# Kernel tuning notes

Hardware: AMD Instinct MI355X
Metric: run time of the kernel (lower is better)

## Reference

```python
import jax, jax.numpy as jnp
import numpy as np

B, S, D_IN = 2, 2048, 1024
H, DA, DH = 16, 64, 64          # num_heads, attention_dim, head_dim (linear_hidden_dim)
EMBED = 1024
KSIZE = 1


def causal_conv1d(x_bsc, w):
    """x_bsc: (B,S,Cin); w: (Cout,Cin,K). Left-pad K-1 -> causal. Returns (B,Cout,S)."""
    k = w.shape[-1]
    x_bcs = jnp.transpose(x_bsc, (0, 2, 1))
    x_bcs = jnp.pad(x_bcs, ((0, 0), (0, 0), (k - 1, 0)))
    return jax.lax.conv_general_dilated(
        x_bcs, w, window_strides=(1,), padding='VALID',
        dimension_numbers=('NCH', 'OIH', 'NCH'))


def setup_inputs() -> dict:
    key = jax.random.key(0)
    ks = jax.random.split(key, 7)
    x = jax.random.normal(ks[0], (B, S, D_IN), dtype=jnp.float32)
    # causal mask: 1 where attended, 0 where masked (masked_fill where ==0)
    attn_mask = jnp.tril(jnp.ones((S, S), dtype=jnp.int32))[None, None]  # (1,1,S,S)
    wq = 0.02 * jax.random.normal(ks[1], (H * DA, D_IN, KSIZE), dtype=jnp.float32)
    wk = 0.02 * jax.random.normal(ks[2], (H * DA, D_IN, KSIZE), dtype=jnp.float32)
    wv = 0.02 * jax.random.normal(ks[3], (H * DH, D_IN, KSIZE), dtype=jnp.float32)
    w_out = 0.02 * jax.random.normal(ks[4], (EMBED, H * DH), dtype=jnp.float32)
    b_out = 0.02 * jax.random.normal(ks[5], (EMBED,), dtype=jnp.float32)
    return {"x": x, "attn_mask": attn_mask, "wq": wq, "wk": wk, "wv": wv,
            "w_out": w_out, "b_out": b_out}


def reference(x, attn_mask, wq, wk, wv, w_out, b_out):
    b, s, _ = x.shape
    scale = DH ** (-0.5)  # NOTE: torch code scales by head_dim, not attention_dim
    q = causal_conv1d(x, wq)  # (B, H*DA, S)
    k = causal_conv1d(x, wk)  # (B, H*DA, S)
    v = causal_conv1d(x, wv)  # (B, H*DH, S)
    q = q.reshape(b, H, DA, s).transpose(0, 1, 3, 2)  # (B,H,S,DA)
    k = k.reshape(b, H, DA, s).transpose(0, 1, 3, 2)
    v = v.reshape(b, H, DH, s).transpose(0, 1, 3, 2)  # (B,H,S,DH)
    scores = scale * jnp.einsum('bhnd,bhmd->bhnm', q, k)
    scores = jnp.where(attn_mask == 0, -jnp.inf, scores)
    probs = jax.nn.softmax(scores, axis=-1)
    context = jnp.einsum('bhnm,bhmd->bhnd', probs, v)  # (B,H,S,DH)
    context = context.transpose(0, 2, 1, 3).reshape(b, s, H * DH)
    return context @ w_out.T + b_out
```

## Files before the change

### kernel.cpp

```cpp
#include <hip/hip_runtime.h>
#include <math.h>


typedef __bf16 bf16;
typedef __bf16 bf16x8 __attribute__((ext_vector_type(8)));
typedef __bf16 bf16x4 __attribute__((ext_vector_type(4)));
typedef float  f32x4  __attribute__((ext_vector_type(4)));

#define MFMA16(a, b, c) __builtin_amdgcn_mfma_f32_16x16x32_bf16((a), (b), (c), 0, 0, 0)

__device__ __forceinline__ void gll16(const void* g, void* l) {
    __builtin_amdgcn_global_load_lds(
        (__attribute__((address_space(1))) unsigned int*)g,
        (__attribute__((address_space(3))) unsigned int*)l, 16, 0, 0);
}

__global__ __launch_bounds__(256) void cvt_all_kernel(
    const float* __restrict__ x,  const float* __restrict__ wq,
    const float* __restrict__ wk, const float* __restrict__ wv,
    const float* __restrict__ wo,
    bf16* __restrict__ xb,  bf16* __restrict__ wqb, bf16* __restrict__ wkb,
    bf16* __restrict__ wvb, bf16* __restrict__ wob)
{
    const int blk = blockIdx.x;
    const float* src; bf16* dst; int off; float scale = 1.f;
    if (blk < 4096)      { src = x;  dst = xb;  off = blk * 1024; }
    else if (blk < 5120) { src = wq; dst = wqb; off = (blk - 4096) * 1024; scale = 0.125f; }
    else if (blk < 6144) { src = wk; dst = wkb; off = (blk - 5120) * 1024; }
    else if (blk < 7168) { src = wv; dst = wvb; off = (blk - 6144) * 1024; }
    else                 { src = wo; dst = wob; off = (blk - 7168) * 1024; }
    const int i = off + threadIdx.x * 4;
    f32x4 v = *(const f32x4*)(src + i);
    bf16x4 o;
    o[0] = (bf16)(v[0] * scale); o[1] = (bf16)(v[1] * scale);
    o[2] = (bf16)(v[2] * scale); o[3] = (bf16)(v[3] * scale);
    *(bf16x4*)(dst + i) = o;
}

__global__ __launch_bounds__(256, 3) void qkv_mfma_kernel(
    const bf16* __restrict__ xb, const bf16* __restrict__ wqb,
    const bf16* __restrict__ wkb, const bf16* __restrict__ wvb,
    bf16* __restrict__ Qb, bf16* __restrict__ Kb, bf16* __restrict__ Vtb)
{
    __shared__ bf16 As[2][128 * 32];
    __shared__ bf16 Bs[2][128 * 32];
    const int mt = blockIdx.x;
    const int nt = blockIdx.y;
    const int which = nt >> 3;
    const bf16* Wm = (which == 0) ? wqb : (which == 1) ? wkb : wvb;

    const int t = threadIdx.x;
    const int w = t >> 6, lane = t & 63, quad = lane >> 4, l16 = lane & 15;
    const int wm = (w >> 1) * 64, wn = (w & 1) * 64;
    const int srow = lane >> 2;
    const int scol = (lane & 3) * 8;

    const bf16* Ab = xb + ((size_t)(mt * 128) + srow) * 1024 + scol;
    const bf16* Bb = Wm + ((size_t)((nt & 7) * 128) + srow) * 1024 + scol;

    f32x4 acc[4][4];
    #pragma unroll
    for (int i = 0; i < 4; i++)
        #pragma unroll
        for (int j = 0; j < 4; j++)
            #pragma unroll
            for (int r = 0; r < 4; r++) acc[i][j][r] = 0.f;

    gll16(Ab + (size_t)(w * 16) * 1024,       As[0] + w * 512);
    gll16(Ab + (size_t)((w + 4) * 16) * 1024, As[0] + (w + 4) * 512);
    gll16(Bb + (size_t)(w * 16) * 1024,       Bs[0] + w * 512);
    gll16(Bb + (size_t)((w + 4) * 16) * 1024, Bs[0] + (w + 4) * 512);

    for (int it = 0; it < 32; it++) {
        const int cur = it & 1, nxt = cur ^ 1;
        __syncthreads();
        if (it < 31) {
            const int kn = it * 32 + 32;
            gll16(Ab + (size_t)(w * 16) * 1024 + kn,       As[nxt] + w * 512);
            gll16(Ab + (size_t)((w + 4) * 16) * 1024 + kn, As[nxt] + (w + 4) * 512);
            gll16(Bb + (size_t)(w * 16) * 1024 + kn,       Bs[nxt] + w * 512);
            gll16(Bb + (size_t)((w + 4) * 16) * 1024 + kn, Bs[nxt] + (w + 4) * 512);
        }
        bf16x8 af[4], bfr[4];
        #pragma unroll
        for (int i = 0; i < 4; i++)
            af[i] = *(const bf16x8*)&As[cur][(wm + i * 16 + l16) * 32 + quad * 8];
        #pragma unroll
        for (int j = 0; j < 4; j++)
            bfr[j] = *(const bf16x8*)&Bs[cur][(wn + j * 16 + l16) * 32 + quad * 8];
        #pragma unroll
        for (int i = 0; i < 4; i++)
            #pragma unroll
            for (int j = 0; j < 4; j++)
                acc[i][j] = MFMA16(af[i], bfr[j], acc[i][j]);
    }

    const int nbase = (nt & 7) * 128 + wn;
    #pragma unroll
    for (int i = 0; i < 4; i++) {
        #pragma unroll
        for (int r = 0; r < 4; r++) {
            const int m = mt * 128 + wm + i * 16 + quad * 4 + r;
            const int bb = m >> 11, s = m & 2047;
            #pragma unroll
            for (int j = 0; j < 4; j++) {
                const int n = nbase + j * 16 + l16;
                const int h = n >> 6, d = n & 63;
                bf16 val = (bf16)acc[i][j][r];
                if (which == 0)
                    Qb[(((size_t)(bb * 16 + h)) * 2048 + s) * 64 + d] = val;
                else if (which == 1)
                    Kb[(((size_t)(bb * 16 + h)) * 2048 + s) * 64 + d] = val;
                else
                    Vtb[(((size_t)(bb * 16 + h)) * 64 + d) * 2048 + s] = val;
            }
        }
    }
}

__global__ __launch_bounds__(256, 2) void attn_mfma_kernel(
    const bf16* __restrict__ Qb, const bf16* __restrict__ Kb,
    const bf16* __restrict__ Vtb, bf16* __restrict__ ctxb)
{
    __shared__ bf16 Qs[128 * 64];
    __shared__ bf16 Ks[2][64 * 64];
    __shared__ bf16 Vts[2][64 * 64];
    __shared__ bf16 Pl[4][32 * 72];

    const int id = blockIdx.x;
    const int bh = id & 31;
    const int g = id >> 5;
    const int qt = (g < 8) ? g : (23 - g);
    const int h = bh & 15, b = bh >> 4;
    const int t = threadIdx.x;
    const int w = t >> 6, lane = t & 63, quad = lane >> 4, l16 = lane & 15;
    const int sr = lane >> 3, sc = lane & 7;

    const size_t hb = (size_t)(b * 16 + h);
    const bf16* Qh = Qb + hb * (2048 * 64);
    const bf16* Kh = Kb + hb * (2048 * 64);
    const bf16* Vh = Vtb + hb * (64 * 2048);

    #pragma unroll
    for (int j = 0; j < 4; j++) {
        const int c = w + 4 * j;
        const int r0 = c * 8 + sr;
        gll16(Qh + (size_t)(qt * 128 + r0) * 64 + (sc ^ sr) * 8, Qs + c * 512);
    }
    {
        const int r0 = w * 8 + sr, r1 = (w + 4) * 8 + sr;
        gll16(Kh + (size_t)r0 * 64 + (sc ^ sr) * 8, Ks[0] + w * 512);
        gll16(Kh + (size_t)r1 * 64 + (sc ^ sr) * 8, Ks[0] + (w + 4) * 512);
        gll16(Vh + (size_t)r0 * 2048 + (sc ^ sr) * 8, Vts[0] + w * 512);
        gll16(Vh + (size_t)r1 * 2048 + (sc ^ sr) * 8, Vts[0] + (w + 4) * 512);
    }
    __syncthreads();

    bf16x8 aq[2][2];
    #pragma unroll
    for (int rt = 0; rt < 2; rt++) {
        const int row = w * 32 + rt * 16 + l16;
        aq[rt][0] = *(const bf16x8*)&Qs[row * 64 + ((quad)     ^ (row & 7)) * 8];
        aq[rt][1] = *(const bf16x8*)&Qs[row * 64 + ((quad + 4) ^ (row & 7)) * 8];
    }

    bf16x8 ones;
    #pragma unroll
    for (int i = 0; i < 8; i++) ones[i] = (bf16)1.0f;

    f32x4 o_acc[2][4], l_acc[2];
    #pragma unroll
    for (int rt = 0; rt < 2; rt++) {
        #pragma unroll
        for (int r = 0; r < 4; r++) l_acc[rt][r] = 0.f;
        #pragma unroll
        for (int dt = 0; dt < 4; dt++)
            #pragma unroll
            for (int r = 0; r < 4; r++) o_acc[rt][dt][r] = 0.f;
    }

    const int ktmax = 2 * qt + 1;
    for (int kt = 0; kt <= ktmax; kt++) {
        const int cur = kt & 1, nxt = cur ^ 1;
        __syncthreads();
        if (kt < ktmax) {
            const int kn = kt + 1;
            const int r0 = w * 8 + sr, r1 = (w + 4) * 8 + sr;
            gll16(Kh + (size_t)(kn * 64 + r0) * 64 + (sc ^ sr) * 8, Ks[nxt] + w * 512);
            gll16(Kh + (size_t)(kn * 64 + r1) * 64 + (sc ^ sr) * 8, Ks[nxt] + (w + 4) * 512);
            gll16(Vh + (size_t)r0 * 2048 + kn * 64 + (sc ^ sr) * 8, Vts[nxt] + w * 512);
            gll16(Vh + (size_t)r1 * 2048 + kn * 64 + (sc ^ sr) * 8, Vts[nxt] + (w + 4) * 512);
        }

        f32x4 sacc[2][4];
        #pragma unroll
        for (int rt = 0; rt < 2; rt++)
            #pragma unroll
            for (int tt = 0; tt < 4; tt++)
                #pragma unroll
                for (int r = 0; r < 4; r++) sacc[rt][tt][r] = 0.f;
        #pragma unroll
        for (int tt = 0; tt < 4; tt++) {
            const int krow = tt * 16 + l16;
            bf16x8 bk0 = *(const bf16x8*)&Ks[cur][krow * 64 + ((quad)     ^ (krow & 7)) * 8];
            bf16x8 bk1 = *(const bf16x8*)&Ks[cur][krow * 64 + ((quad + 4) ^ (krow & 7)) * 8];
            #pragma unroll
            for (int rt = 0; rt < 2; rt++) {
                sacc[rt][tt] = MFMA16(aq[rt][0], bk0, sacc[rt][tt]);
                sacc[rt][tt] = MFMA16(aq[rt][1], bk1, sacc[rt][tt]);
            }
        }

        const bool diag = (kt >= 2 * qt);
        #pragma unroll
        for (int rt = 0; rt < 2; rt++)
            #pragma unroll
            for (int r = 0; r < 4; r++) {
                const int rw = rt * 16 + quad * 4 + r;
                const int qrow = qt * 128 + w * 32 + rw;
                #pragma unroll
                for (int tt = 0; tt < 4; tt++) {
                    float p = __expf(sacc[rt][tt][r]);
                    if (diag && (kt * 64 + tt * 16 + l16) > qrow) p = 0.f;
                    Pl[w][rw * 72 + tt * 16 + l16] = (bf16)p;
                }
            }

        bf16x8 bv[4][2];
        #pragma unroll
        for (int dt = 0; dt < 4; dt++) {
            const int drow = dt * 16 + l16;
            bv[dt][0] = *(const bf16x8*)&Vts[cur][drow * 64 + ((quad)     ^ (drow & 7)) * 8];
            bv[dt][1] = *(const bf16x8*)&Vts[cur][drow * 64 + ((quad + 4) ^ (drow & 7)) * 8];
        }
        #pragma unroll
        for (int rt = 0; rt < 2; rt++) {
            bf16x8 ap0 = *(const bf16x8*)&Pl[w][(rt * 16 + l16) * 72 + quad * 8];
            bf16x8 ap1 = *(const bf16x8*)&Pl[w][(rt * 16 + l16) * 72 + 32 + quad * 8];
            l_acc[rt] = MFMA16(ap0, ones, l_acc[rt]);
            l_acc[rt] = MFMA16(ap1, ones, l_acc[rt]);
            #pragma unroll
            for (int dt = 0; dt < 4; dt++) {
                o_acc[rt][dt] = MFMA16(ap0, bv[dt][0], o_acc[rt][dt]);
                o_acc[rt][dt] = MFMA16(ap1, bv[dt][1], o_acc[rt][dt]);
            }
        }
    }

    #pragma unroll
    for (int rt = 0; rt < 2; rt++)
        #pragma unroll
        for (int r = 0; r < 4; r++) {
            const float inv = 1.f / l_acc[rt][r];
            const int s = qt * 128 + w * 32 + rt * 16 + quad * 4 + r;
            #pragma unroll
            for (int dt = 0; dt < 4; dt++)
                ctxb[((size_t)(b * 2048 + s)) * 1024 + h * 64 + dt * 16 + l16] =
                    (bf16)(o_acc[rt][dt][r] * inv);
        }
}

__global__ __launch_bounds__(256, 2) void oproj_mfma_kernel(
    const bf16* __restrict__ ctxb, const bf16* __restrict__ wob,
    const float* __restrict__ b_out, float* __restrict__ out)
{
    __shared__ bf16 As[2][64 * 32];
    __shared__ bf16 Bs[2][128 * 32];
    const int mt = blockIdx.x;
    const int nt = blockIdx.y;
    const int t = threadIdx.x;
    const int w = t >> 6, lane = t & 63, quad = lane >> 4, l16 = lane & 15;
    const int srow = lane >> 2;
    const int scol = (lane & 3) * 8;

    const bf16* Ab = ctxb + (size_t)(mt * 64 + srow) * 1024 + scol;
    const bf16* Bb = wob + (size_t)(nt * 128 + srow) * 1024 + scol;

    f32x4 acc[8];
    #pragma unroll
    for (int j = 0; j < 8; j++)
        #pragma unroll
        for (int r = 0; r < 4; r++) acc[j][r] = 0.f;

    gll16(Ab + (size_t)(w * 16) * 1024,       As[0] + w * 512);
    gll16(Bb + (size_t)(w * 16) * 1024,       Bs[0] + w * 512);
    gll16(Bb + (size_t)((w + 4) * 16) * 1024, Bs[0] + (w + 4) * 512);

    for (int it = 0; it < 32; it++) {
        const int cur = it & 1, nxt = cur ^ 1;
        __syncthreads();
        if (it < 31) {
            const int kn = it * 32 + 32;
            gll16(Ab + (size_t)(w * 16) * 1024 + kn,       As[nxt] + w * 512);
            gll16(Bb + (size_t)(w * 16) * 1024 + kn,       Bs[nxt] + w * 512);
            gll16(Bb + (size_t)((w + 4) * 16) * 1024 + kn, Bs[nxt] + (w + 4) * 512);
        }
        bf16x8 af = *(const bf16x8*)&As[cur][(w * 16 + l16) * 32 + quad * 8];
        #pragma unroll
        for (int j = 0; j < 8; j++) {
            bf16x8 bfr = *(const bf16x8*)&Bs[cur][(j * 16 + l16) * 32 + quad * 8];
            acc[j] = MFMA16(af, bfr, acc[j]);
        }
    }

    #pragma unroll
    for (int j = 0; j < 8; j++)
        #pragma unroll
        for (int r = 0; r < 4; r++) {
            const int m = mt * 64 + w * 16 + quad * 4 + r;
            const int n = nt * 128 + j * 16 + l16;
            out[(size_t)m * 1024 + n] = acc[j][r] + b_out[n];
        }
}

extern "C" void kernel_launch(void* const* d_in, const int* in_sizes, int n_in,
                              void* d_out, int out_size, void* d_ws, size_t ws_size,
                              hipStream_t stream)
{
    const float* x     = (const float*)d_in[0];
    const float* wq    = (const float*)d_in[2];
    const float* wk    = (const float*)d_in[3];
    const float* wv    = (const float*)d_in[4];
    const float* w_out = (const float*)d_in[5];
    const float* b_out = (const float*)d_in[6];
    float* out = (float*)d_out;

    char* ws = (char*)d_ws;
    bf16* xb   = (bf16*)(ws);
    bf16* wqb  = (bf16*)(ws + (8u  << 20));
    bf16* wkb  = (bf16*)(ws + (10u << 20));
    bf16* wvb  = (bf16*)(ws + (12u << 20));
    bf16* wob  = (bf16*)(ws + (14u << 20));
    bf16* Qb   = (bf16*)(ws + (16u << 20));
    bf16* Kb   = (bf16*)(ws + (24u << 20));
    bf16* Vtb  = (bf16*)(ws + (32u << 20));
    bf16* ctxb = (bf16*)(ws + (40u << 20));

    cvt_all_kernel<<<8192, 256, 0, stream>>>(x, wq, wk, wv, w_out,
                                             xb, wqb, wkb, wvb, wob);
    qkv_mfma_kernel<<<dim3(32, 24), 256, 0, stream>>>(xb, wqb, wkb, wvb, Qb, Kb, Vtb);
    attn_mfma_kernel<<<512, 256, 0, stream>>>(Qb, Kb, Vtb, ctxb);
    oproj_mfma_kernel<<<dim3(64, 8), 256, 0, stream>>>(ctxb, wob, b_out, out);
}
```

Baseline: 215.3 us.

## Transpose QK^T MFMA, use exp2 with folded log2e, vectorize P and V stores

Folds log2(e) into the Q weight scale so softmax can use the hardware exp2 instruction. It computes S^T by swapping the MFMA operands, which lets each lane write four contiguous P values as one vector store into a smaller per-wave LDS buffer. Q is now loaded straight from global memory into registers, which removes its LDS staging and a barrier. The V-transpose epilogue writes packed bf16x4 vectors, and the q-tile to block mapping is remapped for load balance. The P buffer is now reused across the two row tiles, which may need extra wave-level ordering and adds some risk of hazards.

```diff
diff --git a/kernel.cpp b/kernel.cpp
--- a/kernel.cpp
+++ b/kernel.cpp
@@ -25,7 +25,8 @@
     const int blk = blockIdx.x;
     const float* src; bf16* dst; int off; float scale = 1.f;
     if (blk < 4096)      { src = x;  dst = xb;  off = blk * 1024; }
-    else if (blk < 5120) { src = wq; dst = wqb; off = (blk - 4096) * 1024; scale = 0.125f; }
+    else if (blk < 5120) { src = wq; dst = wqb; off = (blk - 4096) * 1024;
+                           scale = 0.18033688011112042f; }
     else if (blk < 6144) { src = wk; dst = wkb; off = (blk - 5120) * 1024; }
     else if (blk < 7168) { src = wv; dst = wvb; off = (blk - 6144) * 1024; }
     else                 { src = wo; dst = wob; off = (blk - 7168) * 1024; }
@@ -96,23 +97,36 @@
     }
 
     const int nbase = (nt & 7) * 128 + wn;
-    #pragma unroll
-    for (int i = 0; i < 4; i++) {
-        #pragma unroll
-        for (int r = 0; r < 4; r++) {
-            const int m = mt * 128 + wm + i * 16 + quad * 4 + r;
-            const int bb = m >> 11, s = m & 2047;
+    if (which == 2) {
+        #pragma unroll
+        for (int i = 0; i < 4; i++) {
+            const int m0 = mt * 128 + wm + i * 16 + quad * 4;
+            const int bb = m0 >> 11, s0 = m0 & 2047;
             #pragma unroll
             for (int j = 0; j < 4; j++) {
                 const int n = nbase + j * 16 + l16;
                 const int h = n >> 6, d = n & 63;
-                bf16 val = (bf16)acc[i][j][r];
-                if (which == 0)
-                    Qb[(((size_t)(bb * 16 + h)) * 2048 + s) * 64 + d] = val;
-                else if (which == 1)
-                    Kb[(((size_t)(bb * 16 + h)) * 2048 + s) * 64 + d] = val;
-                else
-                    Vtb[(((size_t)(bb * 16 + h)) * 64 + d) * 2048 + s] = val;
+                bf16x4 pk;
+                #pragma unroll
+                for (int r = 0; r < 4; r++) pk[r] = (bf16)acc[i][j][r];
+                *(bf16x4*)&Vtb[(((size_t)(bb * 16 + h)) * 64 + d) * 2048 + s0] = pk;
+            }
+        }
+    } else {
+        bf16* Out = (which == 0) ? Qb : Kb;
+        #pragma unroll
+        for (int i = 0; i < 4; i++) {
+            #pragma unroll
+            for (int r = 0; r < 4; r++) {
+                const int m = mt * 128 + wm + i * 16 + quad * 4 + r;
+                const int bb = m >> 11, s = m & 2047;
+                #pragma unroll
+                for (int j = 0; j < 4; j++) {
+                    const int n = nbase + j * 16 + l16;
+                    const int h = n >> 6, d = n & 63;
+                    Out[(((size_t)(bb * 16 + h)) * 2048 + s) * 64 + d] =
+                        (bf16)acc[i][j][r];
+                }
             }
         }
     }
@@ -122,15 +136,16 @@
     const bf16* __restrict__ Qb, const bf16* __restrict__ Kb,
     const bf16* __restrict__ Vtb, bf16* __restrict__ ctxb)
 {
-    __shared__ bf16 Qs[128 * 64];
     __shared__ bf16 Ks[2][64 * 64];
     __shared__ bf16 Vts[2][64 * 64];
-    __shared__ bf16 Pl[4][32 * 72];
+    __shared__ bf16 Pl[4][16 * 72];
 
     const int id = blockIdx.x;
     const int bh = id & 31;
     const int g = id >> 5;
-    const int qt = (g < 8) ? g : (23 - g);
+    const int u = ((g & 7) << 1) | ((bh >> 4) & 1);
+    const int tsel = ((bh >> 3) ^ (g >> 3)) & 1;
+    const int qt = tsel ? (15 - u) : u;
     const int h = bh & 15, b = bh >> 4;
     const int t = threadIdx.x;
     const int w = t >> 6, lane = t & 63, quad = lane >> 4, l16 = lane & 15;
@@ -141,27 +156,20 @@
     const bf16* Kh = Kb + hb * (2048 * 64);
     const bf16* Vh = Vtb + hb * (64 * 2048);
 
-    #pragma unroll
-    for (int j = 0; j < 4; j++) {
-        const int c = w + 4 * j;
-        const int r0 = c * 8 + sr;
-        gll16(Qh + (size_t)(qt * 128 + r0) * 64 + (sc ^ sr) * 8, Qs + c * 512);
-    }
+    bf16x8 qf[2][2];
+    #pragma unroll
+    for (int rt = 0; rt < 2; rt++) {
+        const bf16* Qrow = Qh + (size_t)(qt * 128 + w * 32 + rt * 16 + l16) * 64;
+        qf[rt][0] = *(const bf16x8*)(Qrow + quad * 8);
+        qf[rt][1] = *(const bf16x8*)(Qrow + 32 + quad * 8);
+    }
+
     {
         const int r0 = w * 8 + sr, r1 = (w + 4) * 8 + sr;
         gll16(Kh + (size_t)r0 * 64 + (sc ^ sr) * 8, Ks[0] + w * 512);
         gll16(Kh + (size_t)r1 * 64 + (sc ^ sr) * 8, Ks[0] + (w + 4) * 512);
         gll16(Vh + (size_t)r0 * 2048 + (sc ^ sr) * 8, Vts[0] + w * 512);
         gll16(Vh + (size_t)r1 * 2048 + (sc ^ sr) * 8, Vts[0] + (w + 4) * 512);
-    }
-    __syncthreads();
-
-    bf16x8 aq[2][2];
-    #pragma unroll
-    for (int rt = 0; rt < 2; rt++) {
-        const int row = w * 32 + rt * 16 + l16;
-        aq[rt][0] = *(const bf16x8*)&Qs[row * 64 + ((quad)     ^ (row & 7)) * 8];
-        aq[rt][1] = *(const bf16x8*)&Qs[row * 64 + ((quad + 4) ^ (row & 7)) * 8];
     }
 
     bf16x8 ones;
@@ -202,29 +210,14 @@
         #pragma unroll
         for (int tt = 0; tt < 4; tt++) {
             const int krow = tt * 16 + l16;
-            bf16x8 bk0 = *(const bf16x8*)&Ks[cur][krow * 64 + ((quad)     ^ (krow & 7)) * 8];
-            bf16x8 bk1 = *(const bf16x8*)&Ks[cur][krow * 64 + ((quad + 4) ^ (krow & 7)) * 8];
+            bf16x8 kf0 = *(const bf16x8*)&Ks[cur][krow * 64 + ((quad)     ^ (krow & 7)) * 8];
+            bf16x8 kf1 = *(const bf16x8*)&Ks[cur][krow * 64 + ((quad + 4) ^ (krow & 7)) * 8];
             #pragma unroll
             for (int rt = 0; rt < 2; rt++) {
-                sacc[rt][tt] = MFMA16(aq[rt][0], bk0, sacc[rt][tt]);
-                sacc[rt][tt] = MFMA16(aq[rt][1], bk1, sacc[rt][tt]);
-            }
-        }
-
-        const bool diag = (kt >= 2 * qt);
-        #pragma unroll
-        for (int rt = 0; rt < 2; rt++)
-            #pragma unroll
-            for (int r = 0; r < 4; r++) {
-                const int rw = rt * 16 + quad * 4 + r;
-                const int qrow = qt * 128 + w * 32 + rw;
-                #pragma unroll
-                for (int tt = 0; tt < 4; tt++) {
-                    float p = __expf(sacc[rt][tt][r]);
-                    if (diag && (kt * 64 + tt * 16 + l16) > qrow) p = 0.f;
-                    Pl[w][rw * 72 + tt * 16 + l16] = (bf16)p;
-                }
-            }
+                sacc[rt][tt] = MFMA16(kf0, qf[rt][0], sacc[rt][tt]);
+                sacc[rt][tt] = MFMA16(kf1, qf[rt][1], sacc[rt][tt]);
+            }
+        }
 
         bf16x8 bv[4][2];
         #pragma unroll
@@ -233,10 +226,24 @@
             bv[dt][0] = *(const bf16x8*)&Vts[cur][drow * 64 + ((quad)     ^ (drow & 7)) * 8];
             bv[dt][1] = *(const bf16x8*)&Vts[cur][drow * 64 + ((quad + 4) ^ (drow & 7)) * 8];
         }
+
+        const bool diag = (kt >= 2 * qt);
         #pragma unroll
         for (int rt = 0; rt < 2; rt++) {
-            bf16x8 ap0 = *(const bf16x8*)&Pl[w][(rt * 16 + l16) * 72 + quad * 8];
-            bf16x8 ap1 = *(const bf16x8*)&Pl[w][(rt * 16 + l16) * 72 + 32 + quad * 8];
+            const int qrow = qt * 128 + w * 32 + rt * 16 + l16;
+            #pragma unroll
+            for (int tt = 0; tt < 4; tt++) {
+                bf16x4 pk;
+                #pragma unroll
+                for (int r = 0; r < 4; r++) {
+                    float p = __builtin_amdgcn_exp2f(sacc[rt][tt][r]);
+                    if (diag && (kt * 64 + tt * 16 + quad * 4 + r) > qrow) p = 0.f;
+                    pk[r] = (bf16)p;
+                }
+                *(bf16x4*)&Pl[w][l16 * 72 + tt * 16 + quad * 4] = pk;
+            }
+            bf16x8 ap0 = *(const bf16x8*)&Pl[w][l16 * 72 + quad * 8];
+            bf16x8 ap1 = *(const bf16x8*)&Pl[w][l16 * 72 + 32 + quad * 8];
             l_acc[rt] = MFMA16(ap0, ones, l_acc[rt]);
             l_acc[rt] = MFMA16(ap1, ones, l_acc[rt]);
             #pragma unroll
```

Result: faster. 196.8 us (-8.6%).
